# Optimization experiments

Measured on AMD Instinct MI355X. Metric: run time of the kernel, lower is better.

Reference implementation:

```python
import jax, jax.numpy as jnp
import numpy as np

DIM = 1024
HEADS = 16
HEAD_DIM = DIM // HEADS
SCALE = HEAD_DIM ** -0.5


def setup_inputs() -> dict:
    key = jax.random.key(0)
    ks = jax.random.split(key, 8)
    B, Nx, N, C = 4, 2048, 512, DIM
    s = C ** -0.5
    return {
        "x": jax.random.normal(ks[0], (B, Nx, C), jnp.float32),
        "cls": jax.random.normal(ks[1], (B, N, C), jnp.float32),
        # Linear weights stored as [in, out] (y = x @ W); qkv_bias=False so no biases on kv/q/Lin_att
        "w_kv": jax.random.normal(ks[2], (C, 2 * C), jnp.float32) * s,
        "w_q": jax.random.normal(ks[3], (C, C), jnp.float32) * s,
        "w_la": jax.random.normal(ks[4], (C, HEADS), jnp.float32) * s,
        "w_proj": jax.random.normal(ks[5], (C, C), jnp.float32) * s,
        "b_proj": jax.random.normal(ks[6], (C,), jnp.float32) * 0.01,
        "att_weight": jax.random.normal(ks[7], (1,), jnp.float32) * 0.1,
    }


def reference(x, cls, w_kv, w_q, w_la, w_proj, b_proj, att_weight):
    B, N, C = cls.shape
    Nx = x.shape[1]
    H, D = HEADS, C // HEADS

    # kv projection: [B,Nx,2C] -> k,v each [B,H,Nx,D]
    kv = (x @ w_kv).reshape(B, Nx, 2, H, D)
    k = jnp.transpose(kv[:, :, 0], (0, 2, 1, 3))
    v = jnp.transpose(kv[:, :, 1], (0, 2, 1, 3))
    # q projection: [B,H,N,D]
    q = jnp.transpose((cls @ w_q).reshape(B, N, H, D), (0, 2, 1, 3))

    # attention scores and first softmax: [B,H,N,Nx]
    attn = jax.nn.softmax(jnp.einsum("bhnd,bhmd->bhnm", q, k) * SCALE, axis=-1)

    # learned pooled gate: Lin_att(x) -> [B,Nx,H] -> [B,H,Nx] -> pool over tokens
    g = jnp.transpose(x @ w_la, (0, 2, 1))  # [B,H,Nx]
    g_mean = jnp.mean(g, axis=-1)[:, :, None, None]  # [B,H,1,1]
    g_max = jnp.max(g, axis=-1)[:, :, None, None]
    gate = 0.5 * g_mean + 0.5 * g_max

    # second softmax over gated scores, then blend with original attention
    attn2 = jax.nn.softmax(gate * attn, axis=-1)
    w = att_weight[0]
    attn = w * attn2 + (1.0 - w) * attn

    # AV and output projection
    out = jnp.einsum("bhnm,bhmd->bnhd", attn, v).reshape(B, N, C)
    return out @ w_proj + b_proj
```

## Files before the change

kernel.cpp:

```cpp
#include <hip/hip_runtime.h>
#include <stdint.h>

#define NX 2048
#define NQ 512
#define CDIM 1024
#define NH 16
#define DH 64

typedef __attribute__((ext_vector_type(8))) __bf16 bf16x8;
typedef __attribute__((ext_vector_type(4))) float f32x4;

__device__ __forceinline__ uint16_t f2bf(float f) {
  uint32_t i = __float_as_uint(f);
  uint32_t r = i + 0x7fffu + ((i >> 16) & 1u);
  return (uint16_t)(r >> 16);
}

#define GLD16(g, l)                                                            \
  __builtin_amdgcn_global_load_lds(                                            \
      (const __attribute__((address_space(1))) uint32_t*)(g),                  \
      (__attribute__((address_space(3))) uint32_t*)(l), 16, 0, 0)


__global__ __launch_bounds__(256) void cast2_bf16_kernel(
    const float* __restrict__ s0, uint16_t* __restrict__ d0, int n40,
    const float* __restrict__ s1, uint16_t* __restrict__ d1, int n41) {
  int i = blockIdx.x * blockDim.x + threadIdx.x;
  int stride = gridDim.x * blockDim.x;
  int ntot = n40 + n41;
  for (; i < ntot; i += stride) {
    if (i < n40) {
      float4 v = ((const float4*)s0)[i];
      ushort4 o;
      o.x = f2bf(v.x); o.y = f2bf(v.y); o.z = f2bf(v.z); o.w = f2bf(v.w);
      ((ushort4*)d0)[i] = o;
    } else {
      float4 v = ((const float4*)s1)[i - n40];
      ushort4 o;
      o.x = f2bf(v.x); o.y = f2bf(v.y); o.z = f2bf(v.z); o.w = f2bf(v.w);
      ((ushort4*)d1)[i - n40] = o;
    }
  }
}


__global__ __launch_bounds__(256) void transT_all_kernel(
    const float* __restrict__ w_kv, uint16_t* __restrict__ wkvT,
    const float* __restrict__ w_q, uint16_t* __restrict__ wqT,
    const float* __restrict__ w_proj, uint16_t* __restrict__ wpT) {
  const int z = blockIdx.z;
  const float* src;
  uint16_t* dst;
  int N;
  if (z == 0) { src = w_kv; dst = wkvT; N = 2048; }
  else if (z == 1) { src = w_q; dst = wqT; N = 1024; }
  else { src = w_proj; dst = wpT; N = 1024; }
  const int n0 = blockIdx.x * 64;
  if (n0 >= N) return;
  const int k0 = blockIdx.y * 64;
  __shared__ uint16_t tile[64][65];
  const int tid = threadIdx.x;
#pragma unroll
  for (int it = 0; it < 16; ++it) {
    int idx = it * 256 + tid;
    int r = idx >> 6, c = idx & 63;
    tile[r][c] = f2bf(src[(size_t)(k0 + r) * N + n0 + c]);
  }
  __syncthreads();
#pragma unroll
  for (int it = 0; it < 16; ++it) {
    int idx = it * 256 + tid;
    int r = idx >> 6, c = idx & 63;
    dst[(size_t)(n0 + r) * 1024 + k0 + c] = tile[c][r];
  }
}


__global__ __launch_bounds__(256) void gate_mm_kernel(
    const uint16_t* __restrict__ xh, const float* __restrict__ wla,
    float* __restrict__ gv) {
  __shared__ __align__(16) uint16_t sW[16 * 1024];
  const int tid = threadIdx.x;
  const int wv = tid >> 6;
  const int lane = tid & 63;
  const int lr = lane & 15;
  const int lh = lane >> 4;

#pragma unroll
  for (int it = 0; it < 64; ++it) {
    int i = it * 256 + tid;
    int c = i >> 4, h = i & 15;
    sW[h * 1024 + (((c >> 3) ^ (h & 7)) << 3) + (c & 7)] = f2bf(wla[i]);
  }
  __syncthreads();

  const int rb = blockIdx.x * 64 + wv * 16;
  f32x4 acc = {0.f, 0.f, 0.f, 0.f};
  for (int t = 0; t < 32; ++t) {
    bf16x8 af = *(const bf16x8*)&xh[(size_t)(rb + lr) * 1024 + t * 32 + lh * 8];
    bf16x8 bf = *(const bf16x8*)&sW[lr * 1024 + (((t * 4 + lh) ^ (lr & 7)) << 3)];
    acc = __builtin_amdgcn_mfma_f32_16x16x32_bf16(af, bf, acc, 0, 0, 0);
  }
  int nxg = rb + lh * 4;
  int b = nxg >> 11, nx = nxg & 2047;
  float4 st = {acc[0], acc[1], acc[2], acc[3]};
  *(float4*)&gv[((size_t)b * NH + lr) * NX + nx] = st;
}


__global__ __launch_bounds__(512, 2) void gemm_kv8q(
    const uint16_t* __restrict__ A, const uint16_t* __restrict__ BT,
    uint16_t* __restrict__ outK, uint16_t* __restrict__ outV,
    const uint16_t* __restrict__ Aq, const uint16_t* __restrict__ BTq,
    uint16_t* __restrict__ outQ) {
  __shared__ __align__(16) uint16_t lds[65536];

  const int bx = blockIdx.x, by = blockIdx.y;
  const bool isQ = bx >= 32;
  if (isQ && by >= 4) return;

  const uint16_t* Ap = isQ ? Aq : A;
  const uint16_t* BTp = isQ ? BTq : BT;
  const int rowBase = (isQ ? (bx - 32) : bx) * 256;
  const int colBase = by * 256;

  const int tid = threadIdx.x;
  const int wid = tid >> 6;
  const int lane = tid & 63;
  const int lr = lane & 15;
  const int lh = lane >> 4;
  const int wm = wid >> 2;
  const int wn = wid & 3;

  f32x4 acc[8][4];
#pragma unroll
  for (int m = 0; m < 8; ++m)
#pragma unroll
    for (int n = 0; n < 4; ++n) acc[m][n] = (f32x4){0.f, 0.f, 0.f, 0.f};

  auto stageB = [&](int T, int h) {
    const uint16_t* srcp = BTp + (size_t)(colBase + h * 128) * 1024 + T * 64;
    uint16_t* dst = lds + ((T & 1) * 32768 + 16384 + h * 8192);
#pragma unroll
    for (int it = 0; it < 2; ++it) {
      int s = it * 512 + tid;
      int row = s >> 3, cc = s & 7;
      int sc = cc ^ (row & 7);
      GLD16(srcp + (size_t)row * 1024 + sc * 8,
            dst + ((size_t)it * 512 + wid * 64) * 8);
    }
  };
  auto stageA012 = [&](int T) {
    const uint16_t* srcp = Ap + (size_t)rowBase * 1024 + T * 64;
    uint16_t* dstbase = lds + (T & 1) * 32768;
    int r64 = tid >> 3, cc = tid & 7;
#pragma unroll
    for (int st = 0; st < 3; ++st) {
      int rloc = (r64 < 32) ? (st * 32 + r64) : (96 + st * 32 + r64);
      int sc = cc ^ (rloc & 7);
      int wrow = (wid < 4) ? (st * 32 + wid * 8) : (128 + st * 32 + (wid - 4) * 8);
      GLD16(srcp + (size_t)rloc * 1024 + sc * 8, dstbase + (size_t)wrow * 64);
    }
  };
  auto stageA3 = [&](int T) {
    const uint16_t* srcp = Ap + (size_t)rowBase * 1024 + T * 64;
    uint16_t* dstbase = lds + (T & 1) * 32768;
    int r64 = tid >> 3, cc = tid & 7;
    int rloc = (r64 < 32) ? (96 + r64) : (192 + r64);
    int sc = cc ^ (rloc & 7);
    int wrow = (wid < 4) ? (96 + wid * 8) : (224 + (wid - 4) * 8);
    GLD16(srcp + (size_t)rloc * 1024 + sc * 8, dstbase + (size_t)wrow * 64);
  };

  auto rdA = [&](int p, int m, int kk) -> bf16x8 {
    int r = wm * 128 + m * 16 + lr;
    return *(const bf16x8*)&lds[p * 32768 + r * 64 +
                                (((kk * 4 + lh) ^ (r & 7)) << 3)];
  };
  auto rdB = [&](int p, int n, int kk) -> bf16x8 {
    int r = wn * 64 + n * 16 + lr;
    return *(const bf16x8*)&lds[p * 32768 + 16384 + r * 64 +
                                (((kk * 4 + lh) ^ (r & 7)) << 3)];
  };

  auto tile4 = [&](int t, bool last) {
    const int p = t & 1;
    bf16x8 b[4][2], a0[2], a1[2];
#pragma unroll
    for (int q = 0; q < 4; ++q) {
      if (q == 0) {
#pragma unroll
        for (int n = 0; n < 4; ++n)
#pragma unroll
          for (int kk = 0; kk < 2; ++kk) b[n][kk] = rdB(p, n, kk);
      }
#pragma unroll
      for (int kk = 0; kk < 2; ++kk) {
        a0[kk] = rdA(p, 2 * q, kk);
        a1[kk] = rdA(p, 2 * q + 1, kk);
      }
      if (q == 0) {
        stageA3(t + 1);
      } else if (q == 1) {
        if (!last) stageB(t + 2, 0);
      } else if (q == 2) {
        if (!last) stageB(t + 2, 1);
      } else {
        if (!last) stageA012(t + 2);
        if (last)
          asm volatile("s_waitcnt vmcnt(0)" ::: "memory");
        else
          asm volatile("s_waitcnt vmcnt(7)" ::: "memory");
      }
      __builtin_amdgcn_s_barrier();
      asm volatile("s_waitcnt lgkmcnt(0)" ::: "memory");
      __builtin_amdgcn_sched_barrier(0);
      __builtin_amdgcn_s_setprio(1);
#pragma unroll
      for (int n = 0; n < 4; ++n)
#pragma unroll
        for (int kk = 0; kk < 2; ++kk) {
          acc[2 * q][n] = __builtin_amdgcn_mfma_f32_16x16x32_bf16(
              a0[kk], b[n][kk], acc[2 * q][n], 0, 0, 0);
          acc[2 * q + 1][n] = __builtin_amdgcn_mfma_f32_16x16x32_bf16(
              a1[kk], b[n][kk], acc[2 * q + 1][n], 0, 0, 0);
        }
      __builtin_amdgcn_s_setprio(0);
      __builtin_amdgcn_s_barrier();
      asm volatile("" ::: "memory");
    }
  };

  auto tileEpi = [&](int t) {
    const int p = t & 1;
    bf16x8 b[4][2], a0[2], a1[2];
#pragma unroll
    for (int n = 0; n < 4; ++n)
#pragma unroll
      for (int kk = 0; kk < 2; ++kk) b[n][kk] = rdB(p, n, kk);
#pragma unroll
    for (int q = 0; q < 4; ++q) {
#pragma unroll
      for (int kk = 0; kk < 2; ++kk) {
        a0[kk] = rdA(p, 2 * q, kk);
        a1[kk] = rdA(p, 2 * q + 1, kk);
      }
#pragma unroll
      for (int n = 0; n < 4; ++n)
#pragma unroll
        for (int kk = 0; kk < 2; ++kk) {
          acc[2 * q][n] = __builtin_amdgcn_mfma_f32_16x16x32_bf16(
              a0[kk], b[n][kk], acc[2 * q][n], 0, 0, 0);
          acc[2 * q + 1][n] = __builtin_amdgcn_mfma_f32_16x16x32_bf16(
              a1[kk], b[n][kk], acc[2 * q + 1][n], 0, 0, 0);
        }
    }
  };

  stageB(0, 0); stageB(0, 1); stageA012(0); stageA3(0);
  stageB(1, 0); stageB(1, 1); stageA012(1);
  asm volatile("s_waitcnt vmcnt(7)" ::: "memory");
  __builtin_amdgcn_s_barrier();

  for (int t = 0; t < 14; ++t) tile4(t, false);
  tile4(14, true);
  tileEpi(15);

  if (isQ) {
#pragma unroll
    for (int m = 0; m < 8; ++m) {
      int gr0 = rowBase + wm * 128 + m * 16 + lh * 4;
      int b_ = gr0 >> 9, nq0 = gr0 & 511;
#pragma unroll
      for (int n = 0; n < 4; ++n) {
        int gc = colBase + wn * 64 + n * 16 + lr;
        int hh = gc >> 6, d = gc & 63;
        size_t base = (((size_t)b_ * NH + hh) * NQ + nq0) * DH + d;
#pragma unroll
        for (int j = 0; j < 4; ++j)
          outQ[base + (size_t)j * DH] = f2bf(acc[m][n][j] * 0.125f);
      }
    }
  } else {
#pragma unroll
    for (int m = 0; m < 8; ++m) {
      int gr0 = rowBase + wm * 128 + m * 16 + lh * 4;
      int b_ = gr0 >> 11, nx0 = gr0 & 2047;
#pragma unroll
      for (int n = 0; n < 4; ++n) {
        int gc = colBase + wn * 64 + n * 16 + lr;
        if (gc < 1024) {
          int hh = gc >> 6, d = gc & 63;
          size_t base = (((size_t)b_ * NH + hh) * NX + nx0) * DH + d;
#pragma unroll
          for (int j = 0; j < 4; ++j)
            outK[base + (size_t)j * DH] = f2bf(acc[m][n][j]);
        } else {
          int c2 = gc - 1024;
          int hh = c2 >> 6, d = c2 & 63;
          ushort4 pv;
          pv.x = f2bf(acc[m][n][0]);
          pv.y = f2bf(acc[m][n][1]);
          pv.z = f2bf(acc[m][n][2]);
          pv.w = f2bf(acc[m][n][3]);
          *(ushort4*)&outV[(((size_t)b_ * NH + hh) * DH + d) * NX + nx0] = pv;
        }
      }
    }
  }
}


__global__ __launch_bounds__(256) void gemm_proj(
    const uint16_t* __restrict__ A, const uint16_t* __restrict__ BT,
    float* __restrict__ outF, const float* __restrict__ bias) {
  constexpr int K = 1024;
  __shared__ __align__(16) uint16_t sA[128 * 32];
  __shared__ __align__(16) uint16_t sB[128 * 32];

  const int tid = threadIdx.x;
  const int wv = tid >> 6;
  const int lane = tid & 63;
  const int lr = lane & 15;
  const int lh = lane >> 4;
  const int wm = wv >> 1, wn = wv & 1;
  const int rowBase = blockIdx.x * 128;
  const int colBase = blockIdx.y * 128;

  f32x4 zero4 = {0.f, 0.f, 0.f, 0.f};
  f32x4 acc[4][4];
#pragma unroll
  for (int m = 0; m < 4; ++m)
#pragma unroll
    for (int n = 0; n < 4; ++n) acc[m][n] = zero4;

  for (int k0 = 0; k0 < K; k0 += 32) {
#pragma unroll
    for (int it = 0; it < 2; ++it) {
      int s = it * 256 + tid;
      int row = s >> 2, cc = s & 3;
      int sc = cc ^ ((row >> 1) & 3);
      GLD16(A + (size_t)(rowBase + row) * K + k0 + sc * 8,
            sA + ((size_t)it * 256 + wv * 64) * 8);
      GLD16(BT + (size_t)(colBase + row) * K + k0 + sc * 8,
            sB + ((size_t)it * 256 + wv * 64) * 8);
    }
    __syncthreads();
    bf16x8 af[4], bfr[4];
#pragma unroll
    for (int m = 0; m < 4; ++m) {
      int r = wm * 64 + m * 16 + lr;
      af[m] = *(const bf16x8*)&sA[r * 32 + ((lh ^ ((r >> 1) & 3)) << 3)];
    }
#pragma unroll
    for (int n = 0; n < 4; ++n) {
      int r = wn * 64 + n * 16 + lr;
      bfr[n] = *(const bf16x8*)&sB[r * 32 + ((lh ^ ((r >> 1) & 3)) << 3)];
    }
#pragma unroll
    for (int m = 0; m < 4; ++m)
#pragma unroll
      for (int n = 0; n < 4; ++n)
        acc[m][n] = __builtin_amdgcn_mfma_f32_16x16x32_bf16(af[m], bfr[n],
                                                            acc[m][n], 0, 0, 0);
    __syncthreads();
  }

#pragma unroll
  for (int m = 0; m < 4; ++m) {
    int gr0 = rowBase + wm * 64 + m * 16 + lh * 4;
#pragma unroll
    for (int n = 0; n < 4; ++n) {
      int gc = colBase + wn * 64 + n * 16 + lr;
      float bi = bias[gc];
#pragma unroll
      for (int j = 0; j < 4; ++j)
        outF[(size_t)(gr0 + j) * 1024 + gc] = acc[m][n][j] + bi;
    }
  }
}


__global__ __launch_bounds__(256) void gate2_kernel(
    const float* __restrict__ gv, float* __restrict__ gate) {
  const int bh = blockIdx.x;
  const int tid = threadIdx.x;
  const float* p = gv + (size_t)bh * NX;
  float s = 0.f, mx = -1e30f;
  for (int i = tid; i < NX; i += 256) {
    float v = p[i];
    s += v;
    mx = fmaxf(mx, v);
  }
#pragma unroll
  for (int off = 1; off < 64; off <<= 1) {
    s += __shfl_xor(s, off, 64);
    mx = fmaxf(mx, __shfl_xor(mx, off, 64));
  }
  __shared__ float ss[4], sm[4];
  int wv = tid >> 6, lane = tid & 63;
  if (lane == 0) { ss[wv] = s; sm[wv] = mx; }
  __syncthreads();
  if (tid == 0) {
    float S = ss[0] + ss[1] + ss[2] + ss[3];
    float M = fmaxf(fmaxf(sm[0], sm[1]), fmaxf(sm[2], sm[3]));
    gate[bh] = 0.5f * (S / (float)NX) + 0.5f * M;
  }
}


__global__ __launch_bounds__(256) void vcolsum_kernel(
    const uint16_t* __restrict__ VT, float* __restrict__ vcs) {
  const int bh = blockIdx.x;
  const int wv = threadIdx.x >> 6, lane = threadIdx.x & 63;
#pragma unroll
  for (int dd = 0; dd < 4; ++dd) {
    int d = blockIdx.y * 16 + dd * 4 + wv;
    const uint16_t* row = VT + ((size_t)bh * DH + d) * NX;
    float s = 0.f;
#pragma unroll
    for (int i = 0; i < 4; ++i) {
      bf16x8 v = *(const bf16x8*)&row[(i * 64 + lane) * 8];
#pragma unroll
      for (int j = 0; j < 8; ++j) s += (float)v[j];
    }
#pragma unroll
    for (int off = 1; off < 64; off <<= 1) s += __shfl_xor(s, off, 64);
    if (lane == 0) vcs[bh * DH + d] = s;
  }
}


__global__ __launch_bounds__(256) void attn_kernel(
    const uint16_t* __restrict__ Q, const uint16_t* __restrict__ K,
    const uint16_t* __restrict__ VT, const float* __restrict__ gate,
    const float* __restrict__ attw, const float* __restrict__ vcs,
    uint16_t* __restrict__ ctxh) {
  __shared__ __align__(16) uint16_t sK[128 * 64];
  __shared__ __align__(16) uint16_t sV[64 * 128];
  __shared__ __align__(16) __bf16 sPe[64 * 128];

  const int tid = threadIdx.x;
  const int wv = tid >> 6;
  const int lane = tid & 63;
  const int lr = lane & 15;
  const int lh = lane >> 4;
  const int bh = blockIdx.x;
  const int q0 = blockIdx.y * 64;
  const float g = gate[bh];
  const float w = attw[0];

  const uint16_t* Qb = Q + ((size_t)bh * NQ + q0) * DH;
  const uint16_t* Kb = K + (size_t)bh * NX * DH;
  const uint16_t* Vb = VT + (size_t)bh * DH * NX;

  bf16x8 qa[2];
#pragma unroll
  for (int kk = 0; kk < 2; ++kk)
    qa[kk] = *(const bf16x8*)&Qb[(wv * 16 + lr) * DH + kk * 32 + lh * 8];

  float lp[4] = {0.f, 0.f, 0.f, 0.f};
  f32x4 zero4 = {0.f, 0.f, 0.f, 0.f};
  f32x4 accp[4];
#pragma unroll
  for (int d = 0; d < 4; ++d) accp[d] = zero4;

  for (int kt = 0; kt < 16; ++kt) {
#pragma unroll
    for (int it = 0; it < 4; ++it) {
      int s = it * 256 + tid;
      int row = s >> 3, cc = s & 7;
      int sc = cc ^ (row & 7);
      GLD16(Kb + (size_t)(kt * 128 + row) * DH + sc * 8,
            sK + ((size_t)it * 256 + wv * 64) * 8);
    }
#pragma unroll
    for (int it = 0; it < 4; ++it) {
      int s = it * 256 + tid;
      int row = s >> 4, cc = s & 15;
      int sc = cc ^ (row & 15);
      GLD16(Vb + (size_t)row * NX + kt * 128 + sc * 8,
            sV + ((size_t)it * 256 + wv * 64) * 8);
    }
    __syncthreads();
#pragma unroll
    for (int n = 0; n < 8; ++n) {
      f32x4 a4 = {0.f, 0.f, 0.f, 0.f};
      int r = n * 16 + lr;
#pragma unroll
      for (int kk = 0; kk < 2; ++kk) {
        bf16x8 kb = *(const bf16x8*)&sK[r * 64 + (((kk * 4 + lh) ^ (r & 7)) << 3)];
        a4 = __builtin_amdgcn_mfma_f32_16x16x32_bf16(qa[kk], kb, a4, 0, 0, 0);
      }
#pragma unroll
      for (int j = 0; j < 4; ++j) {
        float e = __expf(a4[j]);
        lp[j] += e;
        int qr = wv * 16 + lh * 4 + j;
        int key = n * 16 + lr;
        int idx = qr * 128 + ((((key >> 3) ^ (qr & 15))) << 3) + (key & 7);
        sPe[idx] = (__bf16)e;
      }
    }
    __syncthreads();
    const int prow = wv * 16 + lr;
#pragma unroll
    for (int kk = 0; kk < 4; ++kk) {
      int pidx = prow * 128 + (((kk * 4 + lh) ^ (prow & 15)) << 3);
      bf16x8 pe = *(const bf16x8*)&sPe[pidx];
#pragma unroll
      for (int df = 0; df < 4; ++df) {
        int vr = df * 16 + lr;
        bf16x8 vb = *(const bf16x8*)&sV[vr * 128 + (((kk * 4 + lh) ^ (vr & 15)) << 3)];
        accp[df] = __builtin_amdgcn_mfma_f32_16x16x32_bf16(pe, vb, accp[df], 0, 0, 0);
      }
    }
    __syncthreads();
  }
#pragma unroll
  for (int off = 1; off < 16; off <<= 1)
#pragma unroll
    for (int j = 0; j < 4; ++j) lp[j] += __shfl_xor(lp[j], off, 64);

  const int b = bh >> 4, h = bh & 15;
  const float c1 = w / ((float)NX + g);
  const float c2 = w * g / ((float)NX + g) + (1.f - w);
  float rl[4];
#pragma unroll
  for (int j = 0; j < 4; ++j) rl[j] = 1.f / lp[j];
#pragma unroll
  for (int df = 0; df < 4; ++df) {
    int d = df * 16 + lr;
    float cv = vcs[bh * DH + d];
#pragma unroll
    for (int j = 0; j < 4; ++j) {
      int qr = q0 + wv * 16 + lh * 4 + j;
      float p = accp[df][j] * rl[j];
      ctxh[(((size_t)b * NQ + qr) * NH + h) * DH + d] = f2bf(c1 * cv + c2 * p);
    }
  }
}


extern "C" void kernel_launch(void* const* d_in, const int* in_sizes, int n_in,
                              void* d_out, int out_size, void* d_ws,
                              size_t ws_size, hipStream_t stream) {
  const float* x = (const float*)d_in[0];
  const float* cls = (const float*)d_in[1];
  const float* w_kv = (const float*)d_in[2];
  const float* w_q = (const float*)d_in[3];
  const float* w_la = (const float*)d_in[4];
  const float* w_proj = (const float*)d_in[5];
  const float* b_proj = (const float*)d_in[6];
  const float* att_w = (const float*)d_in[7];
  float* out = (float*)d_out;

  char* ws = (char*)d_ws;
  size_t off = 0;
  auto alloc = [&](size_t bytes) {
    void* p = ws + off;
    off += (bytes + 255) & ~(size_t)255;
    return p;
  };
  uint16_t* xh = (uint16_t*)alloc(4ull * NX * CDIM * 2);
  uint16_t* ch = (uint16_t*)alloc(4ull * NQ * CDIM * 2);
  uint16_t* wkvT = (uint16_t*)alloc(2048ull * 1024 * 2);
  uint16_t* wqT = (uint16_t*)alloc(1024ull * 1024 * 2);
  uint16_t* wpT = (uint16_t*)alloc(1024ull * 1024 * 2);
  uint16_t* kbf = (uint16_t*)alloc(4ull * NH * NX * DH * 2);
  uint16_t* vT = (uint16_t*)alloc(4ull * NH * DH * NX * 2);
  uint16_t* qbf = (uint16_t*)alloc(4ull * NH * NQ * DH * 2);
  float* gv = (float*)alloc(4ull * NH * NX * 4);
  float* gate = (float*)alloc(1024);
  float* vcs = (float*)alloc(4ull * NH * DH * 4);
  uint16_t* ctxh = (uint16_t*)alloc(4ull * NQ * CDIM * 2);

  cast2_bf16_kernel<<<2048, 256, 0, stream>>>(x, xh, 4 * NX * CDIM / 4,
                                              cls, ch, 4 * NQ * CDIM / 4);
  transT_all_kernel<<<dim3(32, 16, 3), 256, 0, stream>>>(w_kv, wkvT, w_q, wqT,
                                                         w_proj, wpT);

  gate_mm_kernel<<<128, 256, 0, stream>>>(xh, w_la, gv);
  gemm_kv8q<<<dim3(40, 8), 512, 0, stream>>>(xh, wkvT, kbf, vT, ch, wqT, qbf);

  gate2_kernel<<<64, 256, 0, stream>>>(gv, gate);
  vcolsum_kernel<<<dim3(64, 4), 256, 0, stream>>>(vT, vcs);

  attn_kernel<<<dim3(64, 8), 256, 0, stream>>>(qbf, kbf, vT, gate, att_w, vcs, ctxh);

  gemm_proj<<<dim3(16, 8), 256, 0, stream>>>(ctxh, wpT, out, b_proj);
}
```

Before: 157.8 us.

## Move Q projection out of KV GEMM into fused gate/Q auxiliary kernel

The Q projection GEMM moves out of the big 256x256-tile KV kernel and into the small gate kernel, which now also runs 128 blocks of a simple 128x128-tile GEMM. The KV kernel's grid becomes a clean 32x8 of 256 blocks with no early-exit blocks and no per-block branching. The aim is to balance work across kernels and CUs so the KV launch fills the device evenly. In exchange, Q uses a simpler, less pipelined GEMM and the aux kernel's runtime grows.

```diff
diff --git a/kernel.cpp b/kernel.cpp
--- a/kernel.cpp
+++ b/kernel.cpp
@@ -76,53 +76,106 @@
 }
 
 
-__global__ __launch_bounds__(256) void gate_mm_kernel(
-    const uint16_t* __restrict__ xh, const float* __restrict__ wla,
-    float* __restrict__ gv) {
-  __shared__ __align__(16) uint16_t sW[16 * 1024];
+__global__ __launch_bounds__(256) void aux_mm_kernel(
+    const uint16_t* __restrict__ ch, const uint16_t* __restrict__ wqT,
+    uint16_t* __restrict__ qbf, const uint16_t* __restrict__ xh,
+    const float* __restrict__ wla, float* __restrict__ gv) {
+  __shared__ __align__(16) uint16_t smem[16 * 1024];
   const int tid = threadIdx.x;
   const int wv = tid >> 6;
   const int lane = tid & 63;
   const int lr = lane & 15;
   const int lh = lane >> 4;
 
-#pragma unroll
-  for (int it = 0; it < 64; ++it) {
-    int i = it * 256 + tid;
-    int c = i >> 4, h = i & 15;
-    sW[h * 1024 + (((c >> 3) ^ (h & 7)) << 3) + (c & 7)] = f2bf(wla[i]);
-  }
-  __syncthreads();
-
-  const int rb = blockIdx.x * 64 + wv * 16;
-  f32x4 acc = {0.f, 0.f, 0.f, 0.f};
-  for (int t = 0; t < 32; ++t) {
-    bf16x8 af = *(const bf16x8*)&xh[(size_t)(rb + lr) * 1024 + t * 32 + lh * 8];
-    bf16x8 bf = *(const bf16x8*)&sW[lr * 1024 + (((t * 4 + lh) ^ (lr & 7)) << 3)];
-    acc = __builtin_amdgcn_mfma_f32_16x16x32_bf16(af, bf, acc, 0, 0, 0);
-  }
-  int nxg = rb + lh * 4;
-  int b = nxg >> 11, nx = nxg & 2047;
-  float4 st = {acc[0], acc[1], acc[2], acc[3]};
-  *(float4*)&gv[((size_t)b * NH + lr) * NX + nx] = st;
-}
-
-
-__global__ __launch_bounds__(512, 2) void gemm_kv8q(
+  if (blockIdx.x < 128) {
+    uint16_t* sA = smem;
+    uint16_t* sB = smem + 128 * 32;
+    const int wm = wv >> 1, wn = wv & 1;
+    const int rowBase = (blockIdx.x & 15) * 128;
+    const int colBase = (blockIdx.x >> 4) * 128;
+
+    f32x4 zero4 = {0.f, 0.f, 0.f, 0.f};
+    f32x4 acc[4][4];
+#pragma unroll
+    for (int m = 0; m < 4; ++m)
+#pragma unroll
+      for (int n = 0; n < 4; ++n) acc[m][n] = zero4;
+
+    for (int k0 = 0; k0 < 1024; k0 += 32) {
+#pragma unroll
+      for (int it = 0; it < 2; ++it) {
+        int s = it * 256 + tid;
+        int row = s >> 2, cc = s & 3;
+        int sc = cc ^ ((row >> 1) & 3);
+        GLD16(ch + (size_t)(rowBase + row) * 1024 + k0 + sc * 8,
+              sA + ((size_t)it * 256 + wv * 64) * 8);
+        GLD16(wqT + (size_t)(colBase + row) * 1024 + k0 + sc * 8,
+              sB + ((size_t)it * 256 + wv * 64) * 8);
+      }
+      __syncthreads();
+      bf16x8 af[4], bfr[4];
+#pragma unroll
+      for (int m = 0; m < 4; ++m) {
+        int r = wm * 64 + m * 16 + lr;
+        af[m] = *(const bf16x8*)&sA[r * 32 + ((lh ^ ((r >> 1) & 3)) << 3)];
+      }
+#pragma unroll
+      for (int n = 0; n < 4; ++n) {
+        int r = wn * 64 + n * 16 + lr;
+        bfr[n] = *(const bf16x8*)&sB[r * 32 + ((lh ^ ((r >> 1) & 3)) << 3)];
+      }
+#pragma unroll
+      for (int m = 0; m < 4; ++m)
+#pragma unroll
+        for (int n = 0; n < 4; ++n)
+          acc[m][n] = __builtin_amdgcn_mfma_f32_16x16x32_bf16(af[m], bfr[n],
+                                                              acc[m][n], 0, 0, 0);
+      __syncthreads();
+    }
+
+#pragma unroll
+    for (int m = 0; m < 4; ++m) {
+      int gr0 = rowBase + wm * 64 + m * 16 + lh * 4;
+      int b = gr0 >> 9, nq0 = gr0 & 511;
+#pragma unroll
+      for (int n = 0; n < 4; ++n) {
+        int gc = colBase + wn * 64 + n * 16 + lr;
+        int hh = gc >> 6, d = gc & 63;
+        size_t base = (((size_t)b * NH + hh) * NQ + nq0) * DH + d;
+#pragma unroll
+        for (int j = 0; j < 4; ++j)
+          qbf[base + (size_t)j * DH] = f2bf(acc[m][n][j] * 0.125f);
+      }
+    }
+  } else {
+    uint16_t* sW = smem;
+#pragma unroll
+    for (int it = 0; it < 64; ++it) {
+      int i = it * 256 + tid;
+      int c = i >> 4, h = i & 15;
+      sW[h * 1024 + (((c >> 3) ^ (h & 7)) << 3) + (c & 7)] = f2bf(wla[i]);
+    }
+    __syncthreads();
+
+    const int rb = (blockIdx.x - 128) * 64 + wv * 16;
+    f32x4 acc = {0.f, 0.f, 0.f, 0.f};
+    for (int t = 0; t < 32; ++t) {
+      bf16x8 af = *(const bf16x8*)&xh[(size_t)(rb + lr) * 1024 + t * 32 + lh * 8];
+      bf16x8 bf = *(const bf16x8*)&sW[lr * 1024 + (((t * 4 + lh) ^ (lr & 7)) << 3)];
+      acc = __builtin_amdgcn_mfma_f32_16x16x32_bf16(af, bf, acc, 0, 0, 0);
+    }
+    int nxg = rb + lh * 4;
+    int b = nxg >> 11, nx = nxg & 2047;
+    float4 st = {acc[0], acc[1], acc[2], acc[3]};
+    *(float4*)&gv[((size_t)b * NH + lr) * NX + nx] = st;
+  }
+}
+
+
+__global__ __launch_bounds__(512, 2) void gemm_kv8(
     const uint16_t* __restrict__ A, const uint16_t* __restrict__ BT,
-    uint16_t* __restrict__ outK, uint16_t* __restrict__ outV,
-    const uint16_t* __restrict__ Aq, const uint16_t* __restrict__ BTq,
-    uint16_t* __restrict__ outQ) {
+    uint16_t* __restrict__ outK, uint16_t* __restrict__ outV) {
   __shared__ __align__(16) uint16_t lds[65536];
-
-  const int bx = blockIdx.x, by = blockIdx.y;
-  const bool isQ = bx >= 32;
-  if (isQ && by >= 4) return;
-
-  const uint16_t* Ap = isQ ? Aq : A;
-  const uint16_t* BTp = isQ ? BTq : BT;
-  const int rowBase = (isQ ? (bx - 32) : bx) * 256;
-  const int colBase = by * 256;
 
   const int tid = threadIdx.x;
   const int wid = tid >> 6;
@@ -131,6 +184,8 @@
   const int lh = lane >> 4;
   const int wm = wid >> 2;
   const int wn = wid & 3;
+  const int rowBase = blockIdx.x * 256;
+  const int colBase = blockIdx.y * 256;
 
   f32x4 acc[8][4];
 #pragma unroll
@@ -139,7 +194,7 @@
     for (int n = 0; n < 4; ++n) acc[m][n] = (f32x4){0.f, 0.f, 0.f, 0.f};
 
   auto stageB = [&](int T, int h) {
-    const uint16_t* srcp = BTp + (size_t)(colBase + h * 128) * 1024 + T * 64;
+    const uint16_t* srcp = BT + (size_t)(colBase + h * 128) * 1024 + T * 64;
     uint16_t* dst = lds + ((T & 1) * 32768 + 16384 + h * 8192);
 #pragma unroll
     for (int it = 0; it < 2; ++it) {
@@ -151,7 +206,7 @@
     }
   };
   auto stageA012 = [&](int T) {
-    const uint16_t* srcp = Ap + (size_t)rowBase * 1024 + T * 64;
+    const uint16_t* srcp = A + (size_t)rowBase * 1024 + T * 64;
     uint16_t* dstbase = lds + (T & 1) * 32768;
     int r64 = tid >> 3, cc = tid & 7;
 #pragma unroll
@@ -163,7 +218,7 @@
     }
   };
   auto stageA3 = [&](int T) {
-    const uint16_t* srcp = Ap + (size_t)rowBase * 1024 + T * 64;
+    const uint16_t* srcp = A + (size_t)rowBase * 1024 + T * 64;
     uint16_t* dstbase = lds + (T & 1) * 32768;
     int r64 = tid >> 3, cc = tid & 7;
     int rloc = (r64 < 32) ? (96 + r64) : (192 + r64);
@@ -266,45 +321,28 @@
   tile4(14, true);
   tileEpi(15);
 
-  if (isQ) {
-#pragma unroll
-    for (int m = 0; m < 8; ++m) {
-      int gr0 = rowBase + wm * 128 + m * 16 + lh * 4;
-      int b_ = gr0 >> 9, nq0 = gr0 & 511;
-#pragma unroll
-      for (int n = 0; n < 4; ++n) {
-        int gc = colBase + wn * 64 + n * 16 + lr;
+#pragma unroll
+  for (int m = 0; m < 8; ++m) {
+    int gr0 = rowBase + wm * 128 + m * 16 + lh * 4;
+    int b_ = gr0 >> 11, nx0 = gr0 & 2047;
+#pragma unroll
+    for (int n = 0; n < 4; ++n) {
+      int gc = colBase + wn * 64 + n * 16 + lr;
+      if (gc < 1024) {
         int hh = gc >> 6, d = gc & 63;
-        size_t base = (((size_t)b_ * NH + hh) * NQ + nq0) * DH + d;
+        size_t base = (((size_t)b_ * NH + hh) * NX + nx0) * DH + d;
 #pragma unroll
         for (int j = 0; j < 4; ++j)
-          outQ[base + (size_t)j * DH] = f2bf(acc[m][n][j] * 0.125f);
-      }
-    }
-  } else {
-#pragma unroll
-    for (int m = 0; m < 8; ++m) {
-      int gr0 = rowBase + wm * 128 + m * 16 + lh * 4;
-      int b_ = gr0 >> 11, nx0 = gr0 & 2047;
-#pragma unroll
-      for (int n = 0; n < 4; ++n) {
-        int gc = colBase + wn * 64 + n * 16 + lr;
-        if (gc < 1024) {
-          int hh = gc >> 6, d = gc & 63;
-          size_t base = (((size_t)b_ * NH + hh) * NX + nx0) * DH + d;
-#pragma unroll
-          for (int j = 0; j < 4; ++j)
-            outK[base + (size_t)j * DH] = f2bf(acc[m][n][j]);
-        } else {
-          int c2 = gc - 1024;
-          int hh = c2 >> 6, d = c2 & 63;
-          ushort4 pv;
-          pv.x = f2bf(acc[m][n][0]);
-          pv.y = f2bf(acc[m][n][1]);
-          pv.z = f2bf(acc[m][n][2]);
-          pv.w = f2bf(acc[m][n][3]);
-          *(ushort4*)&outV[(((size_t)b_ * NH + hh) * DH + d) * NX + nx0] = pv;
-        }
+          outK[base + (size_t)j * DH] = f2bf(acc[m][n][j]);
+      } else {
+        int c2 = gc - 1024;
+        int hh = c2 >> 6, d = c2 & 63;
+        ushort4 pv;
+        pv.x = f2bf(acc[m][n][0]);
+        pv.y = f2bf(acc[m][n][1]);
+        pv.z = f2bf(acc[m][n][2]);
+        pv.w = f2bf(acc[m][n][3]);
+        *(ushort4*)&outV[(((size_t)b_ * NH + hh) * DH + d) * NX + nx0] = pv;
       }
     }
   }
@@ -580,8 +618,8 @@
   transT_all_kernel<<<dim3(32, 16, 3), 256, 0, stream>>>(w_kv, wkvT, w_q, wqT,
                                                          w_proj, wpT);
 
-  gate_mm_kernel<<<128, 256, 0, stream>>>(xh, w_la, gv);
-  gemm_kv8q<<<dim3(40, 8), 512, 0, stream>>>(xh, wkvT, kbf, vT, ch, wqT, qbf);
+  aux_mm_kernel<<<256, 256, 0, stream>>>(ch, wqT, qbf, xh, w_la, gv);
+  gemm_kv8<<<dim3(32, 8), 512, 0, stream>>>(xh, wkvT, kbf, vT);
 
   gate2_kernel<<<64, 256, 0, stream>>>(gv, gate);
   vcolsum_kernel<<<dim3(64, 4), 256, 0, stream>>>(vT, vcs);
```

Result: faster. 142.7 us (-9.6%).
